# Optimization experiments

Measured on AMD Instinct MI355X. Metric: run time of the kernel, lower is better.

The kernel has to match this reference:

```python
import jax, jax.numpy as jnp
import numpy as np

B, L, W, NEG = 128, 80, 5, 5
N, D = 500000, 128
NEG_WEIGHT = 1.0
LAP_NORM = 0.01


def _build_indices():
    # init_emb2pos_index / init_emb2neg_index, vectorized over batch
    posu_w, posv_w = [], []
    for i in range(L):
        for j in range(max(0, i - W), i):
            posu_w.append(j); posv_w.append(i)
        for j in range(i + 1, min(L, i + 1 + W)):
            posu_w.append(j); posv_w.append(i)
    posu_w = np.asarray(posu_w, np.int32)
    posv_w = np.asarray(posv_w, np.int32)
    off = (np.arange(B, dtype=np.int32) * L)[:, None]
    posu = (posu_w[None, :] + off).reshape(-1)
    posv = (posv_w[None, :] + off).reshape(-1)
    negu_w = np.repeat(posv_w, NEG)  # each center index repeated `negative` times
    negu = (negu_w[None, :] + off).reshape(-1)
    pool = np.tile(np.arange(B * L, dtype=np.int32), NEG * W * 2)
    rng = np.random.default_rng(0)
    negv = rng.permutation(pool)[: negu.shape[0]]
    return posu, posv, negu, negv


def setup_inputs() -> dict:
    key = jax.random.key(0)
    k1, k2, k3 = jax.random.split(key, 3)
    initrange = 1.0 / D
    u_weight = jax.random.uniform(k1, (N, D), jnp.float32, -initrange, initrange)
    # original inits v to zeros; use small random values for a nontrivial test
    v_weight = jax.random.normal(k2, (N, D), jnp.float32) * 0.01
    nodes = jax.random.randint(k3, (B, L), 0, N, jnp.int32)
    posu, posv, negu, negv = _build_indices()
    return {
        "u_weight": u_weight,
        "v_weight": v_weight,
        "nodes": nodes,
        "index_emb_posu": jnp.asarray(posu),
        "index_emb_posv": jnp.asarray(posv),
        "index_emb_negu": jnp.asarray(negu),
        "index_emb_negv": jnp.asarray(negv),
    }


def _sigmoid_lut():
    t = jax.nn.sigmoid(jnp.arange(-6.01, 6.01, 0.01, dtype=jnp.float32))
    return t.at[0].set(0.0).at[-1].set(1.0)


def _lut_sigmoid(table, score):
    score = jnp.clip(score, -6.0, 6.0)
    idx = jnp.clip(jnp.floor((score + 6.01) / 0.01).astype(jnp.int32), 0, table.shape[0] - 1)
    return table[idx]


def reference(u_weight, v_weight, nodes, index_emb_posu, index_emb_posv,
              index_emb_negu, index_emb_negv):
    BL = nodes.shape[0] * nodes.shape[1]
    table = _sigmoid_lut()
    flat = nodes.reshape(-1)
    emb_u = u_weight[flat]  # [BL, D]
    emb_v = v_weight[flat]  # [BL, D]

    # positive pairs
    emb_pos_u = emb_u[index_emb_posu]
    emb_pos_v = emb_v[index_emb_posv]
    pos_score = jnp.sum(emb_pos_u * emb_pos_v, axis=1)
    s_pos = (1.0 - _lut_sigmoid(table, pos_score))[:, None]
    grad_u_pos = s_pos * emb_pos_v + LAP_NORM * (emb_pos_v - emb_pos_u)
    grad_v_pos = s_pos * emb_pos_u + LAP_NORM * (emb_pos_u - emb_pos_v)
    grad_u = jax.ops.segment_sum(grad_u_pos, index_emb_posu, num_segments=BL)
    grad_v = jax.ops.segment_sum(grad_v_pos, index_emb_posv, num_segments=BL)

    # negative pairs
    emb_neg_u = emb_u[index_emb_negu]
    emb_neg_v = emb_v[index_emb_negv]
    neg_score = jnp.sum(emb_neg_u * emb_neg_v, axis=1)
    s_neg = (-_lut_sigmoid(table, neg_score))[:, None]
    grad_u = grad_u + jax.ops.segment_sum(NEG_WEIGHT * s_neg * emb_neg_v,
                                          index_emb_negu, num_segments=BL)
    grad_v = grad_v + jax.ops.segment_sum(NEG_WEIGHT * s_neg * emb_neg_u,
                                          index_emb_negv, num_segments=BL)
    return grad_u, grad_v
```

## Files before the change

### kernel.cpp

```cpp
#include <hip/hip_runtime.h>

#define DD  128
#define LL  80
#define WW  5
#define NEGS 5
#define EW  64
#define RW  64

__device__ __forceinline__ int degf(int i) {
    return (i < WW ? i : WW) + ((LL - 1 - i) < WW ? (LL - 1 - i) : WW);
}
__device__ __forceinline__ int prefixf(int i) {
    if (i <= WW) return WW * i + i * (i - 1) / 2;
    if (i <= LL - WW) return 35 + 10 * (i - WW);
    int e = 735;
    for (int t = LL - WW; t < i; ++t) e += (LL + WW - 1) - t;
    return e;
}

__device__ __forceinline__ float rsig(float s) {
    return __builtin_amdgcn_rcpf(1.0f + __expf(-s));
}

__device__ __forceinline__ unsigned f2bf(float f) {
    unsigned u = __float_as_uint(f);
    return (u + 0x7FFFu + ((u >> 16) & 1u)) >> 16;
}

__device__ __forceinline__ void unpack8(uint4 wv, float* fo) {
    fo[0] = __uint_as_float(wv.x << 16);
    fo[1] = __uint_as_float(wv.x & 0xFFFF0000u);
    fo[2] = __uint_as_float(wv.y << 16);
    fo[3] = __uint_as_float(wv.y & 0xFFFF0000u);
    fo[4] = __uint_as_float(wv.z << 16);
    fo[5] = __uint_as_float(wv.z & 0xFFFF0000u);
    fo[6] = __uint_as_float(wv.w << 16);
    fo[7] = __uint_as_float(wv.w & 0xFFFF0000u);
}

__global__ void k_prep(const float* __restrict__ uw, const float* __restrict__ vw,
                       const int* __restrict__ nodes,
                       const int* __restrict__ nu, const int* __restrict__ nv,
                       int BL, int NP, int G_g,
                       unsigned* __restrict__ eu, unsigned* __restrict__ ev,
                       int* __restrict__ cnt, unsigned short* __restrict__ ell,
                       unsigned short* __restrict__ nv16) {
    int b = blockIdx.x;
    int t = threadIdx.x;
    if (b < G_g) {
        int r = b * 8 + (t >> 5);
        if (r >= BL) return;
        int l = t & 31;
        long n = (long)nodes[r];
        float4 a4 = ((const float4*)(uw + n * DD))[l];
        float4 b4 = ((const float4*)(vw + n * DD))[l];
        uint2 pa, pb;
        pa.x = f2bf(a4.x) | (f2bf(a4.y) << 16);
        pa.y = f2bf(a4.z) | (f2bf(a4.w) << 16);
        pb.x = f2bf(b4.x) | (f2bf(b4.y) << 16);
        pb.y = f2bf(b4.z) | (f2bf(b4.w) << 16);
        ((uint2*)(eu + (long)r * RW))[l] = pa;
        ((uint2*)(ev + (long)r * RW))[l] = pb;
    } else {
        int p = (b - G_g) * blockDim.x + t;
        if (p < NP) {
            int vr = nv[p];
            int ur = nu[p];
            nv16[p] = (unsigned short)vr;
            int s = atomicAdd(&cnt[vr], 1);
            if (s < EW) ell[(long)vr * EW + s] = (unsigned short)ur;
        }
    }
}

__global__ __launch_bounds__(256) void k_grad(const unsigned* __restrict__ eu,
                                              const unsigned* __restrict__ ev,
                                              const int* __restrict__ cnt,
                                              const unsigned short* __restrict__ ell,
                                              const unsigned short* __restrict__ nv16,
                                              float* __restrict__ out,
                                              int BL, int ppb) {
    unsigned lane = threadIdx.x & 63u;
    int xcd = blockIdx.x & 7;
    int grp = blockIdx.x >> 3;
    bool is_u = xcd < 4;
    int sidx = grp * 4 + (xcd & 3);
    int r = sidx * 4 + (int)(threadIdx.x >> 6);
    if (r >= BL) return;

    int bb = r / LL;
    int i  = r - bb * LL;
    const uint4* own4 = (const uint4*)(is_u ? eu : ev);
    const uint4* oth4 = (const uint4*)(is_u ? ev : eu);

    unsigned li  = lane & 15u;
    unsigned sub = lane >> 4;

    uint4 ow = own4[(unsigned)r * 16u + li];
    float o[8]; unpack8(ow, o);

    float a[8] = {0.f, 0.f, 0.f, 0.f, 0.f, 0.f, 0.f, 0.f};

    int nlo = i < WW ? i : WW;
    int deg = degf(i);
    int base = bb * LL;

#define PAIR_STEP(xw_, cpos_, valid_)                                        \
    {                                                                        \
        float xv_[8]; unpack8(xw_, xv_);                                     \
        float pd_ = o[0] * xv_[0];                                           \
        pd_ = fmaf(o[1], xv_[1], pd_); pd_ = fmaf(o[2], xv_[2], pd_);        \
        pd_ = fmaf(o[3], xv_[3], pd_); pd_ = fmaf(o[4], xv_[4], pd_);        \
        pd_ = fmaf(o[5], xv_[5], pd_); pd_ = fmaf(o[6], xv_[6], pd_);        \
        pd_ = fmaf(o[7], xv_[7], pd_);                                       \
        pd_ += __shfl_xor(pd_, 1, 16); pd_ += __shfl_xor(pd_, 2, 16);        \
        pd_ += __shfl_xor(pd_, 4, 16); pd_ += __shfl_xor(pd_, 8, 16);        \
        float c_ = (cpos_ ? 1.01f : 0.0f) - rsig(pd_);                       \
        c_ = (valid_) ? c_ : 0.0f;                                           \
        a[0] = fmaf(c_, xv_[0], a[0]); a[1] = fmaf(c_, xv_[1], a[1]);        \
        a[2] = fmaf(c_, xv_[2], a[2]); a[3] = fmaf(c_, xv_[3], a[3]);        \
        a[4] = fmaf(c_, xv_[4], a[4]); a[5] = fmaf(c_, xv_[5], a[5]);        \
        a[6] = fmaf(c_, xv_[6], a[6]); a[7] = fmaf(c_, xv_[7], a[7]);        \
    }

    for (int k = 0; k < deg; k += 4) {
        int t0 = k + (int)sub;
        int tc = t0 < deg - 1 ? t0 : deg - 1;
        int j = (tc < nlo) ? (i - nlo + tc) : (i + 1 + tc - nlo);
        uint4 xw = oth4[(unsigned)(base + j) * 16u + li];
        PAIR_STEP(xw, true, t0 < deg);
    }

    if (is_u) {
        const unsigned short* ids = nv16 + (bb * ppb + NEGS * prefixf(i));
        int nn = NEGS * deg;
        int last = nn - 1;
        int t0 = (int)sub;     t0 = t0 < last ? t0 : last;
        int t1 = (int)sub + 4; t1 = t1 < last ? t1 : last;
        int t2 = (int)sub + 8; t2 = t2 < last ? t2 : last;
        unsigned eA = ids[t2];
        uint4 x0 = oth4[(unsigned)ids[t0] * 16u + li];
        uint4 x1 = oth4[(unsigned)ids[t1] * 16u + li];
        for (int k = 0; k < nn; k += 4) {
            int ti = k + 12 + (int)sub; ti = ti < last ? ti : last;
            unsigned eB = ids[ti];
            uint4 x2 = oth4[eA * 16u + li];
            PAIR_STEP(x0, false, (k + (int)sub) < nn);
            x0 = x1; x1 = x2; eA = eB;
        }
    } else {
        int nn = cnt[r]; nn = nn > EW ? EW : nn;
        if (nn > 0) {
            const unsigned short* lst = ell + (unsigned)r * EW;
            int last = nn - 1;
            int t0 = (int)sub;     t0 = t0 < last ? t0 : last;
            int t1 = (int)sub + 4; t1 = t1 < last ? t1 : last;
            int t2 = (int)sub + 8; t2 = t2 < last ? t2 : last;
            unsigned eA = lst[t2];
            uint4 x0 = oth4[(unsigned)lst[t0] * 16u + li];
            uint4 x1 = oth4[(unsigned)lst[t1] * 16u + li];
            for (int k = 0; k < nn; k += 4) {
                int ti = k + 12 + (int)sub; ti = ti < last ? ti : last;
                unsigned eB = lst[ti];
                uint4 x2 = oth4[eA * 16u + li];
                PAIR_STEP(x0, false, (k + (int)sub) < nn);
                x0 = x1; x1 = x2; eA = eB;
            }
        }
    }
#undef PAIR_STEP

#define XRED(v) v += __shfl_xor(v, 16, 64); v += __shfl_xor(v, 32, 64)
    XRED(a[0]); XRED(a[1]); XRED(a[2]); XRED(a[3]);
    XRED(a[4]); XRED(a[5]); XRED(a[6]); XRED(a[7]);
#undef XRED

    float lam = -0.01f * (float)deg;
#pragma unroll
    for (int k = 0; k < 8; ++k) a[k] = fmaf(lam, o[k], a[k]);

    if (sub == 0) {
        unsigned orow = (unsigned)(is_u ? r : r + BL);
        float4* od = (float4*)out;
        unsigned ob = orow * 32u + li * 2u;
        od[ob + 0] = make_float4(a[0], a[1], a[2], a[3]);
        od[ob + 1] = make_float4(a[4], a[5], a[6], a[7]);
    }
}

extern "C" void kernel_launch(void* const* d_in, const int* in_sizes, int n_in,
                              void* d_out, int out_size, void* d_ws, size_t ws_size,
                              hipStream_t stream) {
    const float* uw  = (const float*)d_in[0];
    const float* vw  = (const float*)d_in[1];
    const int* nodes = (const int*)d_in[2];
    const int* nu    = (const int*)d_in[5];
    const int* nv    = (const int*)d_in[6];
    int BL = in_sizes[2];
    int NP = in_sizes[5];
    float* out = (float*)d_out;

    int B   = BL / LL;
    int ppb = NP / B;

    unsigned* eu = (unsigned*)d_ws;
    unsigned* ev = eu + (size_t)BL * RW;
    int* cnt = (int*)(ev + (size_t)BL * RW);
    unsigned short* ell = (unsigned short*)(cnt + (size_t)BL);
    unsigned short* nv16 = ell + (size_t)BL * EW;

    (void)hipMemsetAsync(cnt, 0, (size_t)BL * sizeof(int), stream);

    int G_g = (BL + 7) / 8;
    int G_b = (NP + 255) / 256;
    k_prep<<<G_g + G_b, 256, 0, stream>>>(uw, vw, nodes, nu, nv,
                                          BL, NP, G_g, eu, ev, cnt, ell, nv16);

    int npb  = (BL + 3) / 4;
    int npb4 = (npb + 3) / 4 * 4;
    k_grad<<<npb4 * 2, 256, 0, stream>>>(eu, ev, cnt, ell, nv16,
                                         out, BL, ppb);
}
```

Measured before the change: 75.59 us.

## Process eight pairs per wave with eight lanes per embedding row

Each wavefront now splits into 8 subgroups of 8 lanes instead of 4 subgroups of 16. Each lane handles 16 bf16 elements, loaded as two uint4. This halves the loop trip count for positive and negative pairs and shortens the dot-product shuffle reduction from four steps to three. In exchange it adds one more cross-subgroup reduction step, raises register pressure, and wastes more lanes on the masked tail when degree is not a multiple of 8.

```diff
diff --git a/kernel.cpp b/kernel.cpp
--- a/kernel.cpp
+++ b/kernel.cpp
@@ -93,98 +93,122 @@
     const uint4* own4 = (const uint4*)(is_u ? eu : ev);
     const uint4* oth4 = (const uint4*)(is_u ? ev : eu);
 
-    unsigned li  = lane & 15u;
-    unsigned sub = lane >> 4;
-
-    uint4 ow = own4[(unsigned)r * 16u + li];
-    float o[8]; unpack8(ow, o);
-
-    float a[8] = {0.f, 0.f, 0.f, 0.f, 0.f, 0.f, 0.f, 0.f};
+    unsigned li  = lane & 7u;
+    unsigned sub = lane >> 3;
+
+    const uint4* orp = own4 + (unsigned)r * 16u + li * 2u;
+    uint4 ow0 = orp[0], ow1 = orp[1];
+    float o[16]; unpack8(ow0, o); unpack8(ow1, o + 8);
+
+    float a[16];
+#pragma unroll
+    for (int k = 0; k < 16; ++k) a[k] = 0.f;
 
     int nlo = i < WW ? i : WW;
     int deg = degf(i);
     int base = bb * LL;
 
-#define PAIR_STEP(xw_, cpos_, valid_)                                        \
+#define PAIR_STEP(xwa_, xwb_, cpos_, valid_)                                 \
     {                                                                        \
-        float xv_[8]; unpack8(xw_, xv_);                                     \
+        float xv_[16]; unpack8(xwa_, xv_); unpack8(xwb_, xv_ + 8);           \
         float pd_ = o[0] * xv_[0];                                           \
-        pd_ = fmaf(o[1], xv_[1], pd_); pd_ = fmaf(o[2], xv_[2], pd_);        \
-        pd_ = fmaf(o[3], xv_[3], pd_); pd_ = fmaf(o[4], xv_[4], pd_);        \
-        pd_ = fmaf(o[5], xv_[5], pd_); pd_ = fmaf(o[6], xv_[6], pd_);        \
-        pd_ = fmaf(o[7], xv_[7], pd_);                                       \
-        pd_ += __shfl_xor(pd_, 1, 16); pd_ += __shfl_xor(pd_, 2, 16);        \
-        pd_ += __shfl_xor(pd_, 4, 16); pd_ += __shfl_xor(pd_, 8, 16);        \
+        pd_ = fmaf(o[1], xv_[1], pd_);  pd_ = fmaf(o[2], xv_[2], pd_);       \
+        pd_ = fmaf(o[3], xv_[3], pd_);  pd_ = fmaf(o[4], xv_[4], pd_);       \
+        pd_ = fmaf(o[5], xv_[5], pd_);  pd_ = fmaf(o[6], xv_[6], pd_);       \
+        pd_ = fmaf(o[7], xv_[7], pd_);  pd_ = fmaf(o[8], xv_[8], pd_);       \
+        pd_ = fmaf(o[9], xv_[9], pd_);  pd_ = fmaf(o[10], xv_[10], pd_);     \
+        pd_ = fmaf(o[11], xv_[11], pd_); pd_ = fmaf(o[12], xv_[12], pd_);    \
+        pd_ = fmaf(o[13], xv_[13], pd_); pd_ = fmaf(o[14], xv_[14], pd_);    \
+        pd_ = fmaf(o[15], xv_[15], pd_);                                     \
+        pd_ += __shfl_xor(pd_, 1, 64);                                       \
+        pd_ += __shfl_xor(pd_, 2, 64);                                       \
+        pd_ += __shfl_xor(pd_, 4, 64);                                       \
         float c_ = (cpos_ ? 1.01f : 0.0f) - rsig(pd_);                       \
         c_ = (valid_) ? c_ : 0.0f;                                           \
-        a[0] = fmaf(c_, xv_[0], a[0]); a[1] = fmaf(c_, xv_[1], a[1]);        \
-        a[2] = fmaf(c_, xv_[2], a[2]); a[3] = fmaf(c_, xv_[3], a[3]);        \
-        a[4] = fmaf(c_, xv_[4], a[4]); a[5] = fmaf(c_, xv_[5], a[5]);        \
-        a[6] = fmaf(c_, xv_[6], a[6]); a[7] = fmaf(c_, xv_[7], a[7]);        \
-    }
-
-    for (int k = 0; k < deg; k += 4) {
+        a[0] = fmaf(c_, xv_[0], a[0]);   a[1] = fmaf(c_, xv_[1], a[1]);      \
+        a[2] = fmaf(c_, xv_[2], a[2]);   a[3] = fmaf(c_, xv_[3], a[3]);      \
+        a[4] = fmaf(c_, xv_[4], a[4]);   a[5] = fmaf(c_, xv_[5], a[5]);      \
+        a[6] = fmaf(c_, xv_[6], a[6]);   a[7] = fmaf(c_, xv_[7], a[7]);      \
+        a[8] = fmaf(c_, xv_[8], a[8]);   a[9] = fmaf(c_, xv_[9], a[9]);      \
+        a[10] = fmaf(c_, xv_[10], a[10]); a[11] = fmaf(c_, xv_[11], a[11]);  \
+        a[12] = fmaf(c_, xv_[12], a[12]); a[13] = fmaf(c_, xv_[13], a[13]);  \
+        a[14] = fmaf(c_, xv_[14], a[14]); a[15] = fmaf(c_, xv_[15], a[15]);  \
+    }
+
+    for (int k = 0; k < deg; k += 8) {
         int t0 = k + (int)sub;
         int tc = t0 < deg - 1 ? t0 : deg - 1;
         int j = (tc < nlo) ? (i - nlo + tc) : (i + 1 + tc - nlo);
-        uint4 xw = oth4[(unsigned)(base + j) * 16u + li];
-        PAIR_STEP(xw, true, t0 < deg);
+        const uint4* xp = oth4 + (unsigned)(base + j) * 16u + li * 2u;
+        uint4 xa = xp[0], xb = xp[1];
+        PAIR_STEP(xa, xb, true, t0 < deg);
     }
 
     if (is_u) {
         const unsigned short* ids = nv16 + (bb * ppb + NEGS * prefixf(i));
         int nn = NEGS * deg;
         int last = nn - 1;
-        int t0 = (int)sub;     t0 = t0 < last ? t0 : last;
-        int t1 = (int)sub + 4; t1 = t1 < last ? t1 : last;
-        int t2 = (int)sub + 8; t2 = t2 < last ? t2 : last;
-        unsigned eA = ids[t2];
-        uint4 x0 = oth4[(unsigned)ids[t0] * 16u + li];
-        uint4 x1 = oth4[(unsigned)ids[t1] * 16u + li];
-        for (int k = 0; k < nn; k += 4) {
-            int ti = k + 12 + (int)sub; ti = ti < last ? ti : last;
+        int t0 = (int)sub;      t0 = t0 < last ? t0 : last;
+        int t1 = (int)sub + 8;  t1 = t1 < last ? t1 : last;
+        int t2 = (int)sub + 16; t2 = t2 < last ? t2 : last;
+        unsigned i0 = ids[t0], i1 = ids[t1], eA = ids[t2];
+        const uint4* p0 = oth4 + i0 * 16u + li * 2u;
+        const uint4* p1 = oth4 + i1 * 16u + li * 2u;
+        uint4 x0a = p0[0], x0b = p0[1];
+        uint4 x1a = p1[0], x1b = p1[1];
+        for (int k = 0; k < nn; k += 8) {
+            int ti = k + 24 + (int)sub; ti = ti < last ? ti : last;
             unsigned eB = ids[ti];
-            uint4 x2 = oth4[eA * 16u + li];
-            PAIR_STEP(x0, false, (k + (int)sub) < nn);
-            x0 = x1; x1 = x2; eA = eB;
+            const uint4* p2 = oth4 + eA * 16u + li * 2u;
+            uint4 x2a = p2[0], x2b = p2[1];
+            PAIR_STEP(x0a, x0b, false, (k + (int)sub) < nn);
+            x0a = x1a; x0b = x1b; x1a = x2a; x1b = x2b; eA = eB;
         }
     } else {
         int nn = cnt[r]; nn = nn > EW ? EW : nn;
         if (nn > 0) {
             const unsigned short* lst = ell + (unsigned)r * EW;
             int last = nn - 1;
-            int t0 = (int)sub;     t0 = t0 < last ? t0 : last;
-            int t1 = (int)sub + 4; t1 = t1 < last ? t1 : last;
-            int t2 = (int)sub + 8; t2 = t2 < last ? t2 : last;
-            unsigned eA = lst[t2];
-            uint4 x0 = oth4[(unsigned)lst[t0] * 16u + li];
-            uint4 x1 = oth4[(unsigned)lst[t1] * 16u + li];
-            for (int k = 0; k < nn; k += 4) {
-                int ti = k + 12 + (int)sub; ti = ti < last ? ti : last;
+            int t0 = (int)sub;      t0 = t0 < last ? t0 : last;
+            int t1 = (int)sub + 8;  t1 = t1 < last ? t1 : last;
+            int t2 = (int)sub + 16; t2 = t2 < last ? t2 : last;
+            unsigned i0 = lst[t0], i1 = lst[t1], eA = lst[t2];
+            const uint4* p0 = oth4 + i0 * 16u + li * 2u;
+            const uint4* p1 = oth4 + i1 * 16u + li * 2u;
+            uint4 x0a = p0[0], x0b = p0[1];
+            uint4 x1a = p1[0], x1b = p1[1];
+            for (int k = 0; k < nn; k += 8) {
+                int ti = k + 24 + (int)sub; ti = ti < last ? ti : last;
                 unsigned eB = lst[ti];
-                uint4 x2 = oth4[eA * 16u + li];
-                PAIR_STEP(x0, false, (k + (int)sub) < nn);
-                x0 = x1; x1 = x2; eA = eB;
+                const uint4* p2 = oth4 + eA * 16u + li * 2u;
+                uint4 x2a = p2[0], x2b = p2[1];
+                PAIR_STEP(x0a, x0b, false, (k + (int)sub) < nn);
+                x0a = x1a; x0b = x1b; x1a = x2a; x1b = x2b; eA = eB;
             }
         }
     }
 #undef PAIR_STEP
 
-#define XRED(v) v += __shfl_xor(v, 16, 64); v += __shfl_xor(v, 32, 64)
-    XRED(a[0]); XRED(a[1]); XRED(a[2]); XRED(a[3]);
-    XRED(a[4]); XRED(a[5]); XRED(a[6]); XRED(a[7]);
+#define XRED(v) v += __shfl_xor(v, 8, 64); v += __shfl_xor(v, 16, 64); \
+                v += __shfl_xor(v, 32, 64)
+    XRED(a[0]);  XRED(a[1]);  XRED(a[2]);  XRED(a[3]);
+    XRED(a[4]);  XRED(a[5]);  XRED(a[6]);  XRED(a[7]);
+    XRED(a[8]);  XRED(a[9]);  XRED(a[10]); XRED(a[11]);
+    XRED(a[12]); XRED(a[13]); XRED(a[14]); XRED(a[15]);
 #undef XRED
 
     float lam = -0.01f * (float)deg;
 #pragma unroll
-    for (int k = 0; k < 8; ++k) a[k] = fmaf(lam, o[k], a[k]);
+    for (int k = 0; k < 16; ++k) a[k] = fmaf(lam, o[k], a[k]);
 
     if (sub == 0) {
-        unsigned orow = (unsigned)(is_u ? r : r + BL);
+        unsigned orw = (unsigned)(is_u ? r : r + BL);
         float4* od = (float4*)out;
-        unsigned ob = orow * 32u + li * 2u;
-        od[ob + 0] = make_float4(a[0], a[1], a[2], a[3]);
-        od[ob + 1] = make_float4(a[4], a[5], a[6], a[7]);
+        unsigned ob = orw * 32u + li * 4u;
+        od[ob + 0] = make_float4(a[0],  a[1],  a[2],  a[3]);
+        od[ob + 1] = make_float4(a[4],  a[5],  a[6],  a[7]);
+        od[ob + 2] = make_float4(a[8],  a[9],  a[10], a[11]);
+        od[ob + 3] = make_float4(a[12], a[13], a[14], a[15]);
     }
 }
 
```

Result: slower. 77.37 us (+2.3%).

## Fuse memset, prep and gradient kernels into one cooperative persistent kernel

Applied to the files above, without the earlier changes.

Replaces the memset plus two separate kernel launches with a single cooperative kernel of fixed grid size. It uses grid-wide syncs between the counter-zeroing, bf16 gather/ELL-build and gradient phases, and the gradient phase now loops persistently over rows. The intent is to remove per-launch overhead and inter-kernel gaps. In exchange it pays the cost of grid barriers and reduces the parallelism available in each phase.

```diff
diff --git a/kernel.cpp b/kernel.cpp
--- a/kernel.cpp
+++ b/kernel.cpp
@@ -1,4 +1,7 @@
 #include <hip/hip_runtime.h>
+#include <hip/hip_cooperative_groups.h>
+
+namespace cg = cooperative_groups;
 
 #define DD  128
 #define LL  80
@@ -6,6 +9,7 @@
 #define NEGS 5
 #define EW  64
 #define RW  64
+#define GRID 1024
 
 __device__ __forceinline__ int degf(int i) {
     return (i < WW ? i : WW) + ((LL - 1 - i) < WW ? (LL - 1 - i) : WW);
@@ -38,32 +42,44 @@
     fo[7] = __uint_as_float(wv.w & 0xFFFF0000u);
 }
 
-__global__ void k_prep(const float* __restrict__ uw, const float* __restrict__ vw,
-                       const int* __restrict__ nodes,
-                       const int* __restrict__ nu, const int* __restrict__ nv,
-                       int BL, int NP, int G_g,
-                       unsigned* __restrict__ eu, unsigned* __restrict__ ev,
-                       int* __restrict__ cnt, unsigned short* __restrict__ ell,
-                       unsigned short* __restrict__ nv16) {
-    int b = blockIdx.x;
-    int t = threadIdx.x;
-    if (b < G_g) {
-        int r = b * 8 + (t >> 5);
-        if (r >= BL) return;
-        int l = t & 31;
-        long n = (long)nodes[r];
-        float4 a4 = ((const float4*)(uw + n * DD))[l];
-        float4 b4 = ((const float4*)(vw + n * DD))[l];
-        uint2 pa, pb;
-        pa.x = f2bf(a4.x) | (f2bf(a4.y) << 16);
-        pa.y = f2bf(a4.z) | (f2bf(a4.w) << 16);
-        pb.x = f2bf(b4.x) | (f2bf(b4.y) << 16);
-        pb.y = f2bf(b4.z) | (f2bf(b4.w) << 16);
-        ((uint2*)(eu + (long)r * RW))[l] = pa;
-        ((uint2*)(ev + (long)r * RW))[l] = pb;
-    } else {
-        int p = (b - G_g) * blockDim.x + t;
-        if (p < NP) {
+__global__ __launch_bounds__(256) void k_fused(
+        const float* __restrict__ uw, const float* __restrict__ vw,
+        const int* __restrict__ nodes,
+        const int* __restrict__ nu, const int* __restrict__ nv,
+        int BL, int NP, int ppb,
+        unsigned* __restrict__ eu, unsigned* __restrict__ ev,
+        int* __restrict__ cnt, unsigned short* __restrict__ ell,
+        unsigned short* __restrict__ nv16,
+        float* __restrict__ out) {
+    cg::grid_group grid = cg::this_grid();
+    int bid = blockIdx.x;
+    int t   = threadIdx.x;
+    int G   = gridDim.x;
+
+    {
+        int idx = bid * 256 + t;
+        if (idx < BL) cnt[idx] = 0;
+    }
+    grid.sync();
+
+    {
+        for (int r0 = bid * 8; r0 < BL; r0 += G * 8) {
+            int r = r0 + (t >> 5);
+            if (r < BL) {
+                int l = t & 31;
+                long n = (long)nodes[r];
+                float4 a4 = ((const float4*)(uw + n * DD))[l];
+                float4 b4 = ((const float4*)(vw + n * DD))[l];
+                uint2 pa, pb;
+                pa.x = f2bf(a4.x) | (f2bf(a4.y) << 16);
+                pa.y = f2bf(a4.z) | (f2bf(a4.w) << 16);
+                pb.x = f2bf(b4.x) | (f2bf(b4.y) << 16);
+                pb.y = f2bf(b4.z) | (f2bf(b4.w) << 16);
+                ((uint2*)(eu + (long)r * RW))[l] = pa;
+                ((uint2*)(ev + (long)r * RW))[l] = pb;
+            }
+        }
+        for (int p = bid * 256 + t; p < NP; p += G * 256) {
             int vr = nv[p];
             int ur = nu[p];
             nv16[p] = (unsigned short)vr;
@@ -71,39 +87,31 @@
             if (s < EW) ell[(long)vr * EW + s] = (unsigned short)ur;
         }
     }
-}
-
-__global__ __launch_bounds__(256) void k_grad(const unsigned* __restrict__ eu,
-                                              const unsigned* __restrict__ ev,
-                                              const int* __restrict__ cnt,
-                                              const unsigned short* __restrict__ ell,
-                                              const unsigned short* __restrict__ nv16,
-                                              float* __restrict__ out,
-                                              int BL, int ppb) {
-    unsigned lane = threadIdx.x & 63u;
-    int xcd = blockIdx.x & 7;
-    int grp = blockIdx.x >> 3;
-    bool is_u = xcd < 4;
-    int sidx = grp * 4 + (xcd & 3);
-    int r = sidx * 4 + (int)(threadIdx.x >> 6);
-    if (r >= BL) return;
-
-    int bb = r / LL;
-    int i  = r - bb * LL;
-    const uint4* own4 = (const uint4*)(is_u ? eu : ev);
-    const uint4* oth4 = (const uint4*)(is_u ? ev : eu);
-
-    unsigned li  = lane & 15u;
-    unsigned sub = lane >> 4;
-
-    uint4 ow = own4[(unsigned)r * 16u + li];
-    float o[8]; unpack8(ow, o);
-
-    float a[8] = {0.f, 0.f, 0.f, 0.f, 0.f, 0.f, 0.f, 0.f};
-
-    int nlo = i < WW ? i : WW;
-    int deg = degf(i);
-    int base = bb * LL;
+    grid.sync();
+
+    {
+        unsigned lane = (unsigned)(t & 63);
+        int xcd = bid & 7;
+        bool is_u = xcd < 4;
+        int sb = (bid >> 3) * 4 + (xcd & 3);
+        int slot = sb * 4 + (t >> 6);
+        int sideSlots = G * 2;
+        const uint4* own4 = (const uint4*)(is_u ? eu : ev);
+        const uint4* oth4 = (const uint4*)(is_u ? ev : eu);
+        unsigned li  = lane & 15u;
+        unsigned sub = lane >> 4;
+
+        for (int r = slot; r < BL; r += sideSlots) {
+            int bb = r / LL;
+            int i  = r - bb * LL;
+
+            uint4 ow = own4[(unsigned)r * 16u + li];
+            float o[8]; unpack8(ow, o);
+            float a[8] = {0.f, 0.f, 0.f, 0.f, 0.f, 0.f, 0.f, 0.f};
+
+            int nlo = i < WW ? i : WW;
+            int deg = degf(i);
+            int base = bb * LL;
 
 #define PAIR_STEP(xw_, cpos_, valid_)                                        \
     {                                                                        \
@@ -123,68 +131,70 @@
         a[6] = fmaf(c_, xv_[6], a[6]); a[7] = fmaf(c_, xv_[7], a[7]);        \
     }
 
-    for (int k = 0; k < deg; k += 4) {
-        int t0 = k + (int)sub;
-        int tc = t0 < deg - 1 ? t0 : deg - 1;
-        int j = (tc < nlo) ? (i - nlo + tc) : (i + 1 + tc - nlo);
-        uint4 xw = oth4[(unsigned)(base + j) * 16u + li];
-        PAIR_STEP(xw, true, t0 < deg);
-    }
-
-    if (is_u) {
-        const unsigned short* ids = nv16 + (bb * ppb + NEGS * prefixf(i));
-        int nn = NEGS * deg;
-        int last = nn - 1;
-        int t0 = (int)sub;     t0 = t0 < last ? t0 : last;
-        int t1 = (int)sub + 4; t1 = t1 < last ? t1 : last;
-        int t2 = (int)sub + 8; t2 = t2 < last ? t2 : last;
-        unsigned eA = ids[t2];
-        uint4 x0 = oth4[(unsigned)ids[t0] * 16u + li];
-        uint4 x1 = oth4[(unsigned)ids[t1] * 16u + li];
-        for (int k = 0; k < nn; k += 4) {
-            int ti = k + 12 + (int)sub; ti = ti < last ? ti : last;
-            unsigned eB = ids[ti];
-            uint4 x2 = oth4[eA * 16u + li];
-            PAIR_STEP(x0, false, (k + (int)sub) < nn);
-            x0 = x1; x1 = x2; eA = eB;
+            for (int k = 0; k < deg; k += 4) {
+                int t0 = k + (int)sub;
+                int tc = t0 < deg - 1 ? t0 : deg - 1;
+                int j = (tc < nlo) ? (i - nlo + tc) : (i + 1 + tc - nlo);
+                uint4 xw = oth4[(unsigned)(base + j) * 16u + li];
+                PAIR_STEP(xw, true, t0 < deg);
+            }
+
+            if (is_u) {
+                const unsigned short* ids = nv16 + (bb * ppb + NEGS * prefixf(i));
+                int nn = NEGS * deg;
+                int last = nn - 1;
+                int t0 = (int)sub;     t0 = t0 < last ? t0 : last;
+                int t1 = (int)sub + 4; t1 = t1 < last ? t1 : last;
+                int t2 = (int)sub + 8; t2 = t2 < last ? t2 : last;
+                unsigned eA = ids[t2];
+                uint4 x0 = oth4[(unsigned)ids[t0] * 16u + li];
+                uint4 x1 = oth4[(unsigned)ids[t1] * 16u + li];
+                for (int k = 0; k < nn; k += 4) {
+                    int ti = k + 12 + (int)sub; ti = ti < last ? ti : last;
+                    unsigned eB = ids[ti];
+                    uint4 x2 = oth4[eA * 16u + li];
+                    PAIR_STEP(x0, false, (k + (int)sub) < nn);
+                    x0 = x1; x1 = x2; eA = eB;
+                }
+            } else {
+                int nn = cnt[r]; nn = nn > EW ? EW : nn;
+                if (nn > 0) {
+                    const unsigned short* lst = ell + (unsigned)r * EW;
+                    int last = nn - 1;
+                    int t0 = (int)sub;     t0 = t0 < last ? t0 : last;
+                    int t1 = (int)sub + 4; t1 = t1 < last ? t1 : last;
+                    int t2 = (int)sub + 8; t2 = t2 < last ? t2 : last;
+                    unsigned eA = lst[t2];
+                    uint4 x0 = oth4[(unsigned)lst[t0] * 16u + li];
+                    uint4 x1 = oth4[(unsigned)lst[t1] * 16u + li];
+                    for (int k = 0; k < nn; k += 4) {
+                        int ti = k + 12 + (int)sub; ti = ti < last ? ti : last;
+                        unsigned eB = lst[ti];
+                        uint4 x2 = oth4[eA * 16u + li];
+                        PAIR_STEP(x0, false, (k + (int)sub) < nn);
+                        x0 = x1; x1 = x2; eA = eB;
+                    }
+                }
+            }
+#undef PAIR_STEP
+
+#define XRED(v) v += __shfl_xor(v, 16, 64); v += __shfl_xor(v, 32, 64)
+            XRED(a[0]); XRED(a[1]); XRED(a[2]); XRED(a[3]);
+            XRED(a[4]); XRED(a[5]); XRED(a[6]); XRED(a[7]);
+#undef XRED
+
+            float lam = -0.01f * (float)deg;
+#pragma unroll
+            for (int k = 0; k < 8; ++k) a[k] = fmaf(lam, o[k], a[k]);
+
+            if (sub == 0) {
+                unsigned orow = (unsigned)(is_u ? r : r + BL);
+                float4* od = (float4*)out;
+                unsigned ob = orow * 32u + li * 2u;
+                od[ob + 0] = make_float4(a[0], a[1], a[2], a[3]);
+                od[ob + 1] = make_float4(a[4], a[5], a[6], a[7]);
+            }
         }
-    } else {
-        int nn = cnt[r]; nn = nn > EW ? EW : nn;
-        if (nn > 0) {
-            const unsigned short* lst = ell + (unsigned)r * EW;
-            int last = nn - 1;
-            int t0 = (int)sub;     t0 = t0 < last ? t0 : last;
-            int t1 = (int)sub + 4; t1 = t1 < last ? t1 : last;
-            int t2 = (int)sub + 8; t2 = t2 < last ? t2 : last;
-            unsigned eA = lst[t2];
-            uint4 x0 = oth4[(unsigned)lst[t0] * 16u + li];
-            uint4 x1 = oth4[(unsigned)lst[t1] * 16u + li];
-            for (int k = 0; k < nn; k += 4) {
-                int ti = k + 12 + (int)sub; ti = ti < last ? ti : last;
-                unsigned eB = lst[ti];
-                uint4 x2 = oth4[eA * 16u + li];
-                PAIR_STEP(x0, false, (k + (int)sub) < nn);
-                x0 = x1; x1 = x2; eA = eB;
-            }
-        }
-    }
-#undef PAIR_STEP
-
-#define XRED(v) v += __shfl_xor(v, 16, 64); v += __shfl_xor(v, 32, 64)
-    XRED(a[0]); XRED(a[1]); XRED(a[2]); XRED(a[3]);
-    XRED(a[4]); XRED(a[5]); XRED(a[6]); XRED(a[7]);
-#undef XRED
-
-    float lam = -0.01f * (float)deg;
-#pragma unroll
-    for (int k = 0; k < 8; ++k) a[k] = fmaf(lam, o[k], a[k]);
-
-    if (sub == 0) {
-        unsigned orow = (unsigned)(is_u ? r : r + BL);
-        float4* od = (float4*)out;
-        unsigned ob = orow * 32u + li * 2u;
-        od[ob + 0] = make_float4(a[0], a[1], a[2], a[3]);
-        od[ob + 1] = make_float4(a[4], a[5], a[6], a[7]);
     }
 }
 
@@ -209,15 +219,10 @@
     unsigned short* ell = (unsigned short*)(cnt + (size_t)BL);
     unsigned short* nv16 = ell + (size_t)BL * EW;
 
-    (void)hipMemsetAsync(cnt, 0, (size_t)BL * sizeof(int), stream);
-
-    int G_g = (BL + 7) / 8;
-    int G_b = (NP + 255) / 256;
-    k_prep<<<G_g + G_b, 256, 0, stream>>>(uw, vw, nodes, nu, nv,
-                                          BL, NP, G_g, eu, ev, cnt, ell, nv16);
-
-    int npb  = (BL + 3) / 4;
-    int npb4 = (npb + 3) / 4 * 4;
-    k_grad<<<npb4 * 2, 256, 0, stream>>>(eu, ev, cnt, ell, nv16,
-                                         out, BL, ppb);
-}
+    void* args[] = { (void*)&uw, (void*)&vw, (void*)&nodes, (void*)&nu,
+                     (void*)&nv, (void*)&BL, (void*)&NP, (void*)&ppb,
+                     (void*)&eu, (void*)&ev, (void*)&cnt, (void*)&ell,
+                     (void*)&nv16, (void*)&out };
+    (void)hipLaunchCooperativeKernel((void*)k_fused, dim3(GRID), dim3(256),
+                                     args, 0, stream);
+}
```

Measured after the change: 257.1 us. 3.4x slower.

## Split prep and grad kernels; fold memset into stage kernel

Applied to the files above, without the earlier changes.

Replaces the hipMemsetAsync with a zeroing branch inside the staging kernel and moves the atomic inverse-index build into its own kernel. The single u/v gradient kernel, which picked its role per block via XCD-based block mapping, becomes two templated kernels (u then v), each launched as a separate grid. The aim is to drop the memset launch and remove the runtime is_u branching. In exchange it adds launches and serialises the u and v gradient work instead of interleaving them, and it drops the XCD-aware block placement.

```diff
diff --git a/kernel.cpp b/kernel.cpp
--- a/kernel.cpp
+++ b/kernel.cpp
@@ -38,67 +38,18 @@
     fo[7] = __uint_as_float(wv.w & 0xFFFF0000u);
 }
 
-__global__ void k_prep(const float* __restrict__ uw, const float* __restrict__ vw,
-                       const int* __restrict__ nodes,
-                       const int* __restrict__ nu, const int* __restrict__ nv,
-                       int BL, int NP, int G_g,
-                       unsigned* __restrict__ eu, unsigned* __restrict__ ev,
-                       int* __restrict__ cnt, unsigned short* __restrict__ ell,
-                       unsigned short* __restrict__ nv16) {
-    int b = blockIdx.x;
-    int t = threadIdx.x;
-    if (b < G_g) {
-        int r = b * 8 + (t >> 5);
-        if (r >= BL) return;
-        int l = t & 31;
-        long n = (long)nodes[r];
-        float4 a4 = ((const float4*)(uw + n * DD))[l];
-        float4 b4 = ((const float4*)(vw + n * DD))[l];
-        uint2 pa, pb;
-        pa.x = f2bf(a4.x) | (f2bf(a4.y) << 16);
-        pa.y = f2bf(a4.z) | (f2bf(a4.w) << 16);
-        pb.x = f2bf(b4.x) | (f2bf(b4.y) << 16);
-        pb.y = f2bf(b4.z) | (f2bf(b4.w) << 16);
-        ((uint2*)(eu + (long)r * RW))[l] = pa;
-        ((uint2*)(ev + (long)r * RW))[l] = pb;
-    } else {
-        int p = (b - G_g) * blockDim.x + t;
-        if (p < NP) {
-            int vr = nv[p];
-            int ur = nu[p];
-            nv16[p] = (unsigned short)vr;
-            int s = atomicAdd(&cnt[vr], 1);
-            if (s < EW) ell[(long)vr * EW + s] = (unsigned short)ur;
-        }
-    }
-}
-
-__global__ __launch_bounds__(256) void k_grad(const unsigned* __restrict__ eu,
-                                              const unsigned* __restrict__ ev,
-                                              const int* __restrict__ cnt,
-                                              const unsigned short* __restrict__ ell,
-                                              const unsigned short* __restrict__ nv16,
-                                              float* __restrict__ out,
-                                              int BL, int ppb) {
-    unsigned lane = threadIdx.x & 63u;
-    int xcd = blockIdx.x & 7;
-    int grp = blockIdx.x >> 3;
-    bool is_u = xcd < 4;
-    int sidx = grp * 4 + (xcd & 3);
-    int r = sidx * 4 + (int)(threadIdx.x >> 6);
-    if (r >= BL) return;
-
+template<bool IS_U>
+__device__ __forceinline__ void grad_row(
+        int r, unsigned li, unsigned sub,
+        const uint4* __restrict__ own4, const uint4* __restrict__ oth4,
+        const int* __restrict__ cnt, const unsigned short* __restrict__ ell,
+        const unsigned short* __restrict__ nv16,
+        float* __restrict__ out, int BL, int ppb) {
     int bb = r / LL;
     int i  = r - bb * LL;
-    const uint4* own4 = (const uint4*)(is_u ? eu : ev);
-    const uint4* oth4 = (const uint4*)(is_u ? ev : eu);
-
-    unsigned li  = lane & 15u;
-    unsigned sub = lane >> 4;
 
     uint4 ow = own4[(unsigned)r * 16u + li];
     float o[8]; unpack8(ow, o);
-
     float a[8] = {0.f, 0.f, 0.f, 0.f, 0.f, 0.f, 0.f, 0.f};
 
     int nlo = i < WW ? i : WW;
@@ -131,7 +82,7 @@
         PAIR_STEP(xw, true, t0 < deg);
     }
 
-    if (is_u) {
+    if (IS_U) {
         const unsigned short* ids = nv16 + (bb * ppb + NEGS * prefixf(i));
         int nn = NEGS * deg;
         int last = nn - 1;
@@ -180,12 +131,83 @@
     for (int k = 0; k < 8; ++k) a[k] = fmaf(lam, o[k], a[k]);
 
     if (sub == 0) {
-        unsigned orow = (unsigned)(is_u ? r : r + BL);
+        unsigned orow = (unsigned)(IS_U ? r : r + BL);
         float4* od = (float4*)out;
         unsigned ob = orow * 32u + li * 2u;
         od[ob + 0] = make_float4(a[0], a[1], a[2], a[3]);
         od[ob + 1] = make_float4(a[4], a[5], a[6], a[7]);
     }
+}
+
+__global__ __launch_bounds__(256) void k_stage(
+        const float* __restrict__ uw, const float* __restrict__ vw,
+        const int* __restrict__ nodes, const int* __restrict__ nv,
+        int BL, int NP, int G_g, int G_c,
+        unsigned* __restrict__ eu, unsigned* __restrict__ ev,
+        unsigned short* __restrict__ nv16, int* __restrict__ cnt) {
+    int b = blockIdx.x;
+    int t = threadIdx.x;
+    if (b < G_g) {
+        int r = b * 8 + (t >> 5);
+        if (r >= BL) return;
+        int l = t & 31;
+        long n = (long)nodes[r];
+        float4 a4 = ((const float4*)(uw + n * DD))[l];
+        float4 b4 = ((const float4*)(vw + n * DD))[l];
+        uint2 pa, pb;
+        pa.x = f2bf(a4.x) | (f2bf(a4.y) << 16);
+        pa.y = f2bf(a4.z) | (f2bf(a4.w) << 16);
+        pb.x = f2bf(b4.x) | (f2bf(b4.y) << 16);
+        pb.y = f2bf(b4.z) | (f2bf(b4.w) << 16);
+        ((uint2*)(eu + (long)r * RW))[l] = pa;
+        ((uint2*)(ev + (long)r * RW))[l] = pb;
+    } else if (b < G_g + G_c) {
+        int idx = (b - G_g) * 256 + t;
+        if (idx < BL) cnt[idx] = 0;
+    } else {
+        int p = (b - G_g - G_c) * 256 + t;
+        if (p < NP) nv16[p] = (unsigned short)nv[p];
+    }
+}
+
+__global__ __launch_bounds__(256) void k_inv(
+        const int* __restrict__ nu, const int* __restrict__ nv, int NP,
+        int* __restrict__ cnt, unsigned short* __restrict__ ell) {
+    int p = blockIdx.x * 256 + threadIdx.x;
+    if (p < NP) {
+        int vr = nv[p];
+        int ur = nu[p];
+        int s = atomicAdd(&cnt[vr], 1);
+        if (s < EW) ell[(long)vr * EW + s] = (unsigned short)ur;
+    }
+}
+
+__global__ __launch_bounds__(256) void k_ugrad(
+        int BL, int ppb,
+        const unsigned short* __restrict__ nv16,
+        const unsigned* __restrict__ eu, const unsigned* __restrict__ ev,
+        float* __restrict__ out) {
+    int r = blockIdx.x * 4 + (threadIdx.x >> 6);
+    if (r >= BL) return;
+    unsigned lane = (unsigned)(threadIdx.x & 63);
+    grad_row<true>(r, lane & 15u, lane >> 4,
+                   (const uint4*)eu, (const uint4*)ev,
+                   (const int*)nullptr, (const unsigned short*)nullptr,
+                   nv16, out, BL, ppb);
+}
+
+__global__ __launch_bounds__(256) void k_vgrad(
+        int BL, int ppb,
+        const int* __restrict__ cnt, const unsigned short* __restrict__ ell,
+        const unsigned* __restrict__ eu, const unsigned* __restrict__ ev,
+        float* __restrict__ out) {
+    int r = blockIdx.x * 4 + (threadIdx.x >> 6);
+    if (r >= BL) return;
+    unsigned lane = (unsigned)(threadIdx.x & 63);
+    grad_row<false>(r, lane & 15u, lane >> 4,
+                    (const uint4*)ev, (const uint4*)eu,
+                    cnt, ell, (const unsigned short*)nullptr,
+                    out, BL, ppb);
 }
 
 extern "C" void kernel_launch(void* const* d_in, const int* in_sizes, int n_in,
@@ -209,15 +231,16 @@
     unsigned short* ell = (unsigned short*)(cnt + (size_t)BL);
     unsigned short* nv16 = ell + (size_t)BL * EW;
 
-    (void)hipMemsetAsync(cnt, 0, (size_t)BL * sizeof(int), stream);
-
     int G_g = (BL + 7) / 8;
-    int G_b = (NP + 255) / 256;
-    k_prep<<<G_g + G_b, 256, 0, stream>>>(uw, vw, nodes, nu, nv,
-                                          BL, NP, G_g, eu, ev, cnt, ell, nv16);
-
-    int npb  = (BL + 3) / 4;
-    int npb4 = (npb + 3) / 4 * 4;
-    k_grad<<<npb4 * 2, 256, 0, stream>>>(eu, ev, cnt, ell, nv16,
-                                         out, BL, ppb);
-}
+    int G_c = (BL + 255) / 256;
+    int G_n = (NP + 255) / 256;
+    k_stage<<<G_g + G_c + G_n, 256, 0, stream>>>(uw, vw, nodes, nv,
+                                                 BL, NP, G_g, G_c,
+                                                 eu, ev, nv16, cnt);
+
+    k_inv<<<(NP + 255) / 256, 256, 0, stream>>>(nu, nv, NP, cnt, ell);
+
+    k_ugrad<<<(BL + 3) / 4, 256, 0, stream>>>(BL, ppb, nv16, eu, ev, out);
+
+    k_vgrad<<<(BL + 3) / 4, 256, 0, stream>>>(BL, ppb, cnt, ell, eu, ev, out);
+}
```

After: 86.89 us. 1.15x slower.
